# Performance work log

Hardware: AMD Instinct MI355X
Metric: run time of the kernel (lower is better)

## Reference

```python
import jax, jax.numpy as jnp
import numpy as np

N_NODES = 50000
N_EDGES = 600000
BAG = 16
VOCAB = 10000
EMB = 128
HID = 128
N_CLASSES = 10
N_GRAPHS = 512
PAD_IDX = 1


def setup_inputs() -> dict:
    key = jax.random.key(0)
    ks = jax.random.split(key, 12)
    x_tokens = jax.random.randint(ks[0], (N_NODES, BAG), 0, VOCAB)
    src = jax.random.randint(ks[1], (N_EDGES,), 0, N_NODES)
    dst = jax.random.randint(ks[2], (N_EDGES,), 0, N_NODES)
    edge_index = jnp.stack([src, dst])
    batch = jnp.sort(jax.random.randint(ks[3], (N_NODES,), 0, N_GRAPHS))
    # rows 0,1 are zero in the original (weights[2:] filled from pretrained vectors)
    emb_table = (jax.random.normal(ks[4], (VOCAB, EMB)) * 0.02).at[:2].set(0.0)
    s = 1.0 / np.sqrt(EMB)
    w1_l = jax.random.normal(ks[5], (HID, EMB)) * s
    b1 = jnp.zeros((HID,), jnp.float32)
    w1_r = jax.random.normal(ks[6], (HID, EMB)) * s
    w2_l = jax.random.normal(ks[7], (HID, HID)) * s
    b2 = jnp.zeros((HID,), jnp.float32)
    w2_r = jax.random.normal(ks[8], (HID, HID)) * s
    w_out = jax.random.normal(ks[9], (N_CLASSES, HID)) * s
    b_out = jnp.zeros((N_CLASSES,), jnp.float32)
    return {"x_tokens": x_tokens, "edge_index": edge_index, "batch": batch,
            "emb_table": emb_table, "w1_l": w1_l, "b1": b1, "w1_r": w1_r,
            "w2_l": w2_l, "b2": b2, "w2_r": w2_r, "w_out": w_out, "b_out": b_out}


def _embedding_bag_mean(tokens, table):
    # nn.EmbeddingBag mode='mean' with padding_idx: padding tokens excluded from mean
    emb = table[tokens]                                  # [N, BAG, D]
    mask = (tokens != PAD_IDX)[..., None].astype(table.dtype)
    total = jnp.sum(emb * mask, axis=1)                  # [N, D]
    cnt = jnp.clip(jnp.sum(mask, axis=1), 1.0)           # [N, 1]
    return total / cnt


def _sage_conv(x, src, dst, w_l, b_l, w_r):
    # PyG SAGEConv: lin_l(mean_{j in N(i)} x_j) + lin_r(x_i); lin_r has no bias
    n = x.shape[0]
    msg_sum = jax.ops.segment_sum(x[src], dst, num_segments=n)           # [N, D]
    deg = jax.ops.segment_sum(jnp.ones((src.shape[0], 1), x.dtype), dst,
                              num_segments=n)                             # [N, 1]
    aggr = msg_sum / jnp.clip(deg, 1.0)
    return aggr @ w_l.T + b_l + x @ w_r.T


def reference(x_tokens, edge_index, batch, emb_table, w1_l, b1, w1_r,
              w2_l, b2, w2_r, w_out, b_out):
    src, dst = edge_index[0], edge_index[1]
    x = _embedding_bag_mean(x_tokens, emb_table)                 # [N, EMB]
    x = jax.nn.relu(_sage_conv(x, src, dst, w1_l, b1, w1_r))     # [N, HID]
    x = jax.nn.relu(_sage_conv(x, src, dst, w2_l, b2, w2_r))     # [N, HID]
    # global_mean_pool over graph ids
    g_sum = jax.ops.segment_sum(x, batch, num_segments=N_GRAPHS)
    g_cnt = jax.ops.segment_sum(jnp.ones((x.shape[0], 1), x.dtype), batch,
                                num_segments=N_GRAPHS)
    g = g_sum / jnp.clip(g_cnt, 1.0)                             # [G, HID]
    return g @ w_out.T + b_out                                   # [G, C]
```

## Files before the change

### kernel.cpp

```cpp
#include <hip/hip_runtime.h>
#include <hip/hip_bf16.h>

#define NN 50000
#define NE 600000
#define BAG 16
#define EMB 128
#define HID 128
#define NC 10
#define NG 512
#define PAD_IDX 1
#define VOCAB 10000
#define SLOTS 64
#define TPAIRS (VOCAB * EMB / 2)
#define WPAIRS (4 * HID * EMB / 2)
#define CONVB ((TPAIRS + WPAIRS + 255) / 256)
#define NCH1 293
#define RANGES 125
#define RNODES 400
#define CSRB (RANGES * 2)
#define EMVB (NN / 16)
#define NTILES ((NN + 127) / 128)
#define ASTR 40

typedef __attribute__((ext_vector_type(8))) short v8s;
typedef __attribute__((ext_vector_type(4))) float v4f;

__device__ __forceinline__ float bflo(unsigned u) { return __uint_as_float(u << 16); }
__device__ __forceinline__ float bfhi(unsigned u) { return __uint_as_float(u & 0xffff0000u); }
__device__ __forceinline__ unsigned short f2bf(float f) {
    unsigned u = __float_as_uint(f);
    return (unsigned short)((u + 0x7fffu + ((u >> 16) & 1u)) >> 16);
}
__device__ __forceinline__ void acc8(float* a, v8s v) {
    unsigned* u = (unsigned*)&v;
#pragma unroll
    for (int j = 0; j < 4; j++) {
        a[2 * j] += bflo(u[j]);
        a[2 * j + 1] += bfhi(u[j]);
    }
}

__global__ __launch_bounds__(256) void k_conv(const int* __restrict__ src,
                                              const int* __restrict__ dst,
                                              unsigned* __restrict__ queue,
                                              int* __restrict__ qcntG,
                                              const float* __restrict__ t,
                                              unsigned short* __restrict__ tb,
                                              const float* __restrict__ w1l,
                                              const float* __restrict__ w1r,
                                              const float* __restrict__ w2l,
                                              const float* __restrict__ w2r,
                                              unsigned short* __restrict__ wbf,
                                              float* __restrict__ gsum,
                                              float* __restrict__ gcnt,
                                              unsigned short* __restrict__ x0,
                                              unsigned short* __restrict__ x1) {
    __shared__ int qcL[RANGES];
    __shared__ unsigned qbL[RANGES * 64];
    int b = blockIdx.x;
    int tid = threadIdx.x;
    if (b < NCH1) {
        for (int i = tid; i < RANGES; i += 256) qcL[i] = 0;
        __syncthreads();
        int e0 = b * 2048 + tid * 8;
        if (e0 < NE) {
            int4 s0 = *((const int4*)(src + e0));
            int4 s1 = *((const int4*)(src + e0) + 1);
            int4 d0 = *((const int4*)(dst + e0));
            int4 d1 = *((const int4*)(dst + e0) + 1);
            int ss[8] = {s0.x, s0.y, s0.z, s0.w, s1.x, s1.y, s1.z, s1.w};
            int dd[8] = {d0.x, d0.y, d0.z, d0.w, d1.x, d1.y, d1.z, d1.w};
#pragma unroll
            for (int j = 0; j < 8; j++) {
                int q = dd[j] / RNODES;
                unsigned pk = ((unsigned)(dd[j] - q * RNODES) << 16) | (unsigned)ss[j];
                int pos = atomicAdd(&qcL[q], 1);
                if (pos < 64) qbL[q * 64 + pos] = pk;
            }
        }
        __syncthreads();
        if (tid < RANGES) {
            int n = qcL[tid];
            if (n > 64) n = 64;
            qcntG[tid * NCH1 + b] = n;
            unsigned* qp = queue + ((size_t)tid * NCH1 + b) * 64;
            for (int k = 0; k < n; k++) qp[k] = qbL[tid * 64 + k];
        }
        return;
    }
    int i = (b - NCH1) * 256 + tid;
    if (i < NG * HID) gsum[i] = 0.f;
    if (i < NG) gcnt[i] = 0.f;
    if (i < 64) {
        ((unsigned*)(x0 + (size_t)NN * EMB))[i] = 0;
        ((unsigned*)(x1 + (size_t)NN * HID))[i] = 0;
    }
    if (i < TPAIRS) {
        float2 v = *(const float2*)(t + (size_t)i * 2);
        unsigned lo = f2bf(v.x), hi = f2bf(v.y);
        *(unsigned*)(tb + (size_t)i * 2) = lo | (hi << 16);
    } else if (i < TPAIRS + WPAIRS) {
        int j = i - TPAIRS;
        int k = j * 2;
        int arr = k >> 14;
        int o = k & 16383;
        const float* w = (arr == 0) ? w1l : (arr == 1) ? w1r : (arr == 2) ? w2l : w2r;
        float2 v = *(const float2*)(w + o);
        unsigned lo = f2bf(v.x), hi = f2bf(v.y);
        *(unsigned*)(wbf + k) = lo | (hi << 16);
    }
}

__global__ __launch_bounds__(256) void k_scatem(const int* __restrict__ qcntG,
                                                const unsigned* __restrict__ queue,
                                                int* __restrict__ cnt,
                                                unsigned short* __restrict__ slots,
                                                const int* __restrict__ tokens,
                                                const unsigned short* __restrict__ table,
                                                unsigned short* __restrict__ x0) {
    __shared__ int cntL[200];
    __shared__ __align__(16) unsigned short slotsL[200 * SLOTS];
    int b = blockIdx.x;
    int tid = threadIdx.x;
    if (b < CSRB) {
        int r = b >> 1, half = b & 1;
        for (int i = tid; i < 200; i += 256) cntL[i] = 0;
        __syncthreads();
        int dlo = half * 200;
        for (int c = tid; c < NCH1; c += 256) {
            int n = qcntG[r * NCH1 + c];
            const unsigned* qp = queue + ((size_t)r * NCH1 + c) * 64;
            for (int k = 0; k < n; k++) {
                unsigned u = qp[k];
                int d2 = (int)(u >> 16) - dlo;
                if ((unsigned)d2 < 200u) {
                    int p = atomicAdd(&cntL[d2], 1);
                    if (p < SLOTS) slotsL[d2 * SLOTS + p] = (unsigned short)(u & 0xffffu);
                }
            }
        }
        __syncthreads();
        for (int i = tid; i < 200; i += 256) {
            int d = cntL[i];
            if (d > SLOTS) d = SLOTS;
            int d8 = (d + 7) & ~7;
            if (d8 > SLOTS) d8 = SLOTS;
            for (int p = d; p < d8; p++) slotsL[i * SLOTS + p] = (unsigned short)NN;
        }
        __syncthreads();
        int nb = r * RNODES + half * 200;
        uint4* gs = (uint4*)(slots + (size_t)nb * SLOTS);
        const uint4* ls = (const uint4*)slotsL;
        for (int i = tid; i < 200 * SLOTS / 8; i += 256) gs[i] = ls[i];
        for (int i = tid; i < 200; i += 256) cnt[nb + i] = cntL[i];
        return;
    }
    int sl = tid & 15;
    int node = (b - CSRB) * 16 + (tid >> 4);
    const int* tp = tokens + node * BAG;
    int tk[16];
    *(int4*)(tk) = *(const int4*)(tp);
    *(int4*)(tk + 4) = *(const int4*)(tp + 4);
    *(int4*)(tk + 8) = *(const int4*)(tp + 8);
    *(int4*)(tk + 12) = *(const int4*)(tp + 12);
    int c = 0;
#pragma unroll
    for (int t = 0; t < BAG; t++) c += (tk[t] != PAD_IDX);
    float a[8];
#pragma unroll
    for (int j = 0; j < 8; j++) a[j] = 0.f;
    v8s v[16];
#pragma unroll
    for (int t = 0; t < 16; t++)
        v[t] = *(const v8s*)(table + (size_t)tk[t] * EMB + sl * 8);
#pragma unroll
    for (int t = 0; t < 16; t++) acc8(a, v[t]);
    float inv = 1.0f / (float)(c > 0 ? c : 1);
    uint4 o;
    o.x = f2bf(a[0] * inv) | ((unsigned)f2bf(a[1] * inv) << 16);
    o.y = f2bf(a[2] * inv) | ((unsigned)f2bf(a[3] * inv) << 16);
    o.z = f2bf(a[4] * inv) | ((unsigned)f2bf(a[5] * inv) << 16);
    o.w = f2bf(a[6] * inv) | ((unsigned)f2bf(a[7] * inv) << 16);
    *(uint4*)(x0 + (size_t)node * EMB + sl * 8) = o;
}

__global__ __launch_bounds__(256) void k_aggr(const unsigned short* __restrict__ x,
                                              const int* __restrict__ cnt,
                                              const unsigned short* __restrict__ slots,
                                              unsigned short* __restrict__ aggr) {
    int wv = threadIdx.x >> 6;
    int lane = threadIdx.x & 63;
    int n0 = (blockIdx.x * 4 + wv) * 2;
    int n1 = n0 + 1;
    int g = lane >> 4, sl = lane & 15;
    int deg0 = cnt[n0], deg1 = cnt[n1];
    int m0 = deg0 > SLOTS ? SLOTS : deg0;
    int m1 = deg1 > SLOTS ? SLOTS : deg1;
    int m80 = (m0 + 7) & ~7;
    int m81 = (m1 + 7) & ~7;
    int idx0 = slots[(size_t)n0 * SLOTS + lane];
    int idx1 = slots[(size_t)n1 * SLOTS + lane];
    float a0[8], a1[8];
#pragma unroll
    for (int j = 0; j < 8; j++) {
        a0[j] = 0.f;
        a1[j] = 0.f;
    }
    int mm = m80 > m81 ? m80 : m81;
#pragma unroll 2
    for (int i = 0; i < mm; i += 8) {
        bool c0 = (i < m80), c1 = (i < m81);
        v8s w0, w1, w2, w3;
        if (c0) {
            int t00 = __shfl(idx0, i + g, 64);
            int t01 = __shfl(idx0, i + 4 + g, 64);
            w0 = *(const v8s*)(x + (size_t)t00 * HID + sl * 8);
            w1 = *(const v8s*)(x + (size_t)t01 * HID + sl * 8);
        }
        if (c1) {
            int t10 = __shfl(idx1, i + g, 64);
            int t11 = __shfl(idx1, i + 4 + g, 64);
            w2 = *(const v8s*)(x + (size_t)t10 * HID + sl * 8);
            w3 = *(const v8s*)(x + (size_t)t11 * HID + sl * 8);
        }
        if (c0) {
            acc8(a0, w0);
            acc8(a0, w1);
        }
        if (c1) {
            acc8(a1, w2);
            acc8(a1, w3);
        }
    }
#pragma unroll
    for (int j = 0; j < 8; j++) {
        a0[j] += __shfl_xor(a0[j], 16, 64);
        a0[j] += __shfl_xor(a0[j], 32, 64);
        a1[j] += __shfl_xor(a1[j], 16, 64);
        a1[j] += __shfl_xor(a1[j], 32, 64);
    }
    if (g == 0) {
        float inv = 1.0f / (float)(deg0 > 0 ? deg0 : 1);
        uint4 o;
        o.x = f2bf(a0[0] * inv) | ((unsigned)f2bf(a0[1] * inv) << 16);
        o.y = f2bf(a0[2] * inv) | ((unsigned)f2bf(a0[3] * inv) << 16);
        o.z = f2bf(a0[4] * inv) | ((unsigned)f2bf(a0[5] * inv) << 16);
        o.w = f2bf(a0[6] * inv) | ((unsigned)f2bf(a0[7] * inv) << 16);
        *(uint4*)(aggr + (size_t)n0 * HID + sl * 8) = o;
    } else if (g == 1) {
        float inv = 1.0f / (float)(deg1 > 0 ? deg1 : 1);
        uint4 o;
        o.x = f2bf(a1[0] * inv) | ((unsigned)f2bf(a1[1] * inv) << 16);
        o.y = f2bf(a1[2] * inv) | ((unsigned)f2bf(a1[3] * inv) << 16);
        o.z = f2bf(a1[4] * inv) | ((unsigned)f2bf(a1[5] * inv) << 16);
        o.w = f2bf(a1[6] * inv) | ((unsigned)f2bf(a1[7] * inv) << 16);
        *(uint4*)(aggr + (size_t)n1 * HID + sl * 8) = o;
    }
}

__device__ __forceinline__ void sage_kloop(int row0, const unsigned short* __restrict__ xa,
                                           const unsigned short* __restrict__ xr,
                                           const unsigned short* __restrict__ wl,
                                           const unsigned short* __restrict__ wr,
                                           unsigned short* As, unsigned short* Bs,
                                           v4f acc[2][8]) {
    int tid = threadIdx.x;
    int wave = tid >> 6, lane = tid & 63;
    int q = lane >> 4, l16 = lane & 15;
    int r0 = tid >> 2, sg = tid & 3;
    int r1 = (tid + 256) >> 2;
    int gr0 = row0 + r0;
    if (gr0 > NN - 1) gr0 = NN - 1;
    int gr1 = row0 + r1;
    if (gr1 > NN - 1) gr1 = NN - 1;
    v8s ra0 = *(const v8s*)(xa + (size_t)gr0 * HID + sg * 8);
    v8s ra1 = *(const v8s*)(xa + (size_t)gr1 * HID + sg * 8);
    v8s rb0 = *(const v8s*)(wl + (size_t)r0 * HID + sg * 8);
    v8s rb1 = *(const v8s*)(wl + (size_t)r1 * HID + sg * 8);
    for (int kc = 0; kc < 8; kc++) {
        __syncthreads();
        *(v8s*)(As + r0 * ASTR + sg * 8) = ra0;
        *(v8s*)(As + r1 * ASTR + sg * 8) = ra1;
        *(v8s*)(Bs + r0 * ASTR + sg * 8) = rb0;
        *(v8s*)(Bs + r1 * ASTR + sg * 8) = rb1;
        __syncthreads();
        if (kc < 7) {
            int kn = kc + 1;
            const unsigned short* Ag = (kn < 4) ? xa : xr;
            const unsigned short* Bg = (kn < 4) ? wl : wr;
            int koff = (kn & 3) * 32;
            ra0 = *(const v8s*)(Ag + (size_t)gr0 * HID + koff + sg * 8);
            ra1 = *(const v8s*)(Ag + (size_t)gr1 * HID + koff + sg * 8);
            rb0 = *(const v8s*)(Bg + (size_t)r0 * HID + koff + sg * 8);
            rb1 = *(const v8s*)(Bg + (size_t)r1 * HID + koff + sg * 8);
        }
        v8s a0 = *(const v8s*)(As + (wave * 32 + l16) * ASTR + q * 8);
        v8s a1 = *(const v8s*)(As + (wave * 32 + 16 + l16) * ASTR + q * 8);
#pragma unroll
        for (int nt = 0; nt < 8; nt++) {
            v8s b = *(const v8s*)(Bs + (nt * 16 + l16) * ASTR + q * 8);
            acc[0][nt] = __builtin_amdgcn_mfma_f32_16x16x32_bf16(a0, b, acc[0][nt], 0, 0, 0);
            acc[1][nt] = __builtin_amdgcn_mfma_f32_16x16x32_bf16(a1, b, acc[1][nt], 0, 0, 0);
        }
    }
    __syncthreads();
}

__global__ __launch_bounds__(256) void k_sage(const unsigned short* __restrict__ xa,
                                              const unsigned short* __restrict__ xr,
                                              const unsigned short* __restrict__ wl,
                                              const unsigned short* __restrict__ wr,
                                              const float* __restrict__ bias,
                                              unsigned short* __restrict__ out) {
    __shared__ unsigned short As[128 * ASTR];
    __shared__ unsigned short Bs[128 * ASTR];
    int row0 = blockIdx.x * 128;
    v4f acc[2][8];
#pragma unroll
    for (int m = 0; m < 2; m++)
#pragma unroll
        for (int n = 0; n < 8; n++) acc[m][n] = (v4f){0.f, 0.f, 0.f, 0.f};
    sage_kloop(row0, xa, xr, wl, wr, As, Bs, acc);
    int tid = threadIdx.x;
    int wave = tid >> 6, lane = tid & 63;
    int q = lane >> 4, l16 = lane & 15;
#pragma unroll
    for (int nt = 0; nt < 8; nt++) {
        int col = nt * 16 + l16;
        float bv = bias[col];
#pragma unroll
        for (int mt = 0; mt < 2; mt++) {
#pragma unroll
            for (int r = 0; r < 4; r++) {
                int row = row0 + wave * 32 + mt * 16 + q * 4 + r;
                if (row < NN) {
                    float v = acc[mt][nt][r] + bv;
                    v = v > 0.f ? v : 0.f;
                    out[(size_t)row * HID + col] = f2bf(v);
                }
            }
        }
    }
}

__global__ __launch_bounds__(256) void k_sagepool(const unsigned short* __restrict__ xa,
                                                  const unsigned short* __restrict__ xr,
                                                  const unsigned short* __restrict__ wl,
                                                  const unsigned short* __restrict__ wr,
                                                  const float* __restrict__ bias,
                                                  const int* __restrict__ batch,
                                                  float* __restrict__ gsum,
                                                  float* __restrict__ gcnt) {
    __shared__ unsigned short smem[128 * 128];
    unsigned short* As = smem;
    unsigned short* Bs = smem + 128 * ASTR;
    int row0 = blockIdx.x * 128;
    v4f acc[2][8];
#pragma unroll
    for (int m = 0; m < 2; m++)
#pragma unroll
        for (int n = 0; n < 8; n++) acc[m][n] = (v4f){0.f, 0.f, 0.f, 0.f};
    sage_kloop(row0, xa, xr, wl, wr, As, Bs, acc);
    int tid = threadIdx.x;
    int wave = tid >> 6, lane = tid & 63;
    int q = lane >> 4, l16 = lane & 15;
#pragma unroll
    for (int nt = 0; nt < 8; nt++) {
        int col = nt * 16 + l16;
        float bv = bias[col];
#pragma unroll
        for (int mt = 0; mt < 2; mt++) {
#pragma unroll
            for (int r = 0; r < 4; r++) {
                int rl = wave * 32 + mt * 16 + q * 4 + r;
                float v = acc[mt][nt][r] + bv;
                v = v > 0.f ? v : 0.f;
                smem[rl * 128 + col] = f2bf(v);
            }
        }
    }
    __syncthreads();
    if (tid < 128) {
        int col = tid;
        int end = NN - row0;
        if (end > 128) end = 128;
        int cur = batch[row0];
        float acc_p = 0.f;
        int c = 0;
        for (int i = 0; i < end; i++) {
            int b = batch[row0 + i];
            if (b != cur) {
                atomicAdd(&gsum[cur * HID + col], acc_p);
                if (col == 0) atomicAdd(&gcnt[cur], (float)c);
                acc_p = 0.f;
                c = 0;
                cur = b;
            }
            acc_p += __uint_as_float(((unsigned)smem[i * 128 + col]) << 16);
            c++;
        }
        atomicAdd(&gsum[cur * HID + col], acc_p);
        if (col == 0) atomicAdd(&gcnt[cur], (float)c);
    }
}

__global__ __launch_bounds__(128) void k_final(const float* __restrict__ gsum,
                                               const float* __restrict__ gcnt,
                                               const float* __restrict__ w_out,
                                               const float* __restrict__ b_out,
                                               float* __restrict__ out) {
    __shared__ float mean[HID];
    int g = blockIdx.x, tid = threadIdx.x;
    mean[tid] = gsum[g * HID + tid] / fmaxf(gcnt[g], 1.0f);
    __syncthreads();
    if (tid < NC) {
        float s = b_out[tid];
#pragma unroll 16
        for (int d = 0; d < HID; d++) s += mean[d] * w_out[tid * HID + d];
        out[g * NC + tid] = s;
    }
}

extern "C" void kernel_launch(void* const* d_in, const int* in_sizes, int n_in,
                              void* d_out, int out_size, void* d_ws, size_t ws_size,
                              hipStream_t stream) {
    const int* x_tokens = (const int*)d_in[0];
    const int* edge = (const int*)d_in[1];
    const int* batch = (const int*)d_in[2];
    const float* emb_table = (const float*)d_in[3];
    const float* w1l = (const float*)d_in[4];
    const float* b1 = (const float*)d_in[5];
    const float* w1r = (const float*)d_in[6];
    const float* w2l = (const float*)d_in[7];
    const float* b2 = (const float*)d_in[8];
    const float* w2r = (const float*)d_in[9];
    const float* w_out = (const float*)d_in[10];
    const float* b_out = (const float*)d_in[11];
    float* out = (float*)d_out;

    char* ws = (char*)d_ws;
    size_t off = 0;
    auto alloc = [&](size_t bytes) {
        void* p = ws + off;
        off += (bytes + 255) & ~(size_t)255;
        return p;
    };
    int* cnt = (int*)alloc(NN * 4);
    unsigned short* slots = (unsigned short*)alloc((size_t)NN * SLOTS * 2);
    unsigned short* wbf = (unsigned short*)alloc(4 * HID * EMB * 2);
    float* gsum = (float*)alloc(NG * HID * 4);
    float* gcnt = (float*)alloc(NG * 4);
    unsigned short* x0 = (unsigned short*)alloc((size_t)(NN + 1) * EMB * 2);
    unsigned short* x1 = (unsigned short*)alloc((size_t)(NN + 1) * HID * 2);
    unsigned short* aggrb = (unsigned short*)alloc((size_t)NN * HID * 2);
    unsigned* queue = (unsigned*)alloc((size_t)RANGES * NCH1 * 64 * 4);
    int* qcntG = (int*)alloc((size_t)RANGES * NCH1 * 4);
    unsigned short* table_bf = x1;

    const int* srcp = edge;
    const int* dstp = edge + NE;

    k_conv<<<NCH1 + CONVB, 256, 0, stream>>>(srcp, dstp, queue, qcntG, emb_table,
                                             table_bf, w1l, w1r, w2l, w2r, wbf,
                                             gsum, gcnt, x0, x1);
    k_scatem<<<CSRB + EMVB, 256, 0, stream>>>(qcntG, queue, cnt, slots, x_tokens,
                                              table_bf, x0);
    k_aggr<<<NN / 8, 256, 0, stream>>>(x0, cnt, slots, aggrb);
    k_sage<<<NTILES, 256, 0, stream>>>(aggrb, x0, wbf, wbf + 16384, b1, x1);
    k_aggr<<<NN / 8, 256, 0, stream>>>(x1, cnt, slots, aggrb);
    k_sagepool<<<NTILES, 256, 0, stream>>>(aggrb, x1, wbf + 32768, wbf + 49152, b2,
                                           batch, gsum, gcnt);
    k_final<<<NG, 128, 0, stream>>>(gsum, gcnt, w_out, b_out, out);
}
```

Baseline: 195.6 us.

## Fuse all stages into one cooperative persistent kernel with grid syncs

Replaces the seven separate kernel launches with one cooperative persistent kernel. Each stage becomes a device function, blocks loop over its work units in grid-stride order, and the stages are separated by grid-wide syncs. The goal is to remove launch gaps and kernel-boundary drain between the many short stages. The risks are grid-sync overhead, occupancy capped by a fixed 33KB shared allocation and launch bounds of 3, and worse load balance in stages that have few tiles; the multi-kernel path remains as a fallback.

```diff
diff --git a/kernel.cpp b/kernel.cpp
--- a/kernel.cpp
+++ b/kernel.cpp
@@ -1,4 +1,5 @@
 #include <hip/hip_runtime.h>
+#include <hip/hip_cooperative_groups.h>
 #include <hip/hip_bf16.h>
 
 #define NN 50000
@@ -40,124 +41,132 @@
     }
 }
 
-__global__ __launch_bounds__(256) void k_conv(const int* __restrict__ src,
-                                              const int* __restrict__ dst,
-                                              unsigned* __restrict__ queue,
-                                              int* __restrict__ qcntG,
-                                              const float* __restrict__ t,
-                                              unsigned short* __restrict__ tb,
-                                              const float* __restrict__ w1l,
-                                              const float* __restrict__ w1r,
-                                              const float* __restrict__ w2l,
-                                              const float* __restrict__ w2r,
-                                              unsigned short* __restrict__ wbf,
-                                              float* __restrict__ gsum,
-                                              float* __restrict__ gcnt,
-                                              unsigned short* __restrict__ x0,
-                                              unsigned short* __restrict__ x1) {
-    __shared__ int qcL[RANGES];
-    __shared__ unsigned qbL[RANGES * 64];
-    int b = blockIdx.x;
-    int tid = threadIdx.x;
-    if (b < NCH1) {
-        for (int i = tid; i < RANGES; i += 256) qcL[i] = 0;
-        __syncthreads();
-        int e0 = b * 2048 + tid * 8;
-        if (e0 < NE) {
-            int4 s0 = *((const int4*)(src + e0));
-            int4 s1 = *((const int4*)(src + e0) + 1);
-            int4 d0 = *((const int4*)(dst + e0));
-            int4 d1 = *((const int4*)(dst + e0) + 1);
-            int ss[8] = {s0.x, s0.y, s0.z, s0.w, s1.x, s1.y, s1.z, s1.w};
-            int dd[8] = {d0.x, d0.y, d0.z, d0.w, d1.x, d1.y, d1.z, d1.w};
-#pragma unroll
-            for (int j = 0; j < 8; j++) {
-                int q = dd[j] / RNODES;
-                unsigned pk = ((unsigned)(dd[j] - q * RNODES) << 16) | (unsigned)ss[j];
-                int pos = atomicAdd(&qcL[q], 1);
-                if (pos < 64) qbL[q * 64 + pos] = pk;
-            }
-        }
-        __syncthreads();
-        if (tid < RANGES) {
-            int n = qcL[tid];
-            if (n > 64) n = 64;
-            qcntG[tid * NCH1 + b] = n;
-            unsigned* qp = queue + ((size_t)tid * NCH1 + b) * 64;
-            for (int k = 0; k < n; k++) qp[k] = qbL[tid * 64 + k];
-        }
-        return;
-    }
-    int i = (b - NCH1) * 256 + tid;
-    if (i < NG * HID) gsum[i] = 0.f;
-    if (i < NG) gcnt[i] = 0.f;
+struct MegaArgs {
+    const int* src;
+    const int* dst;
+    unsigned* queue;
+    int* qcntG;
+    const float* emb_table;
+    unsigned short* table_bf;
+    const float* w1l;
+    const float* w1r;
+    const float* w2l;
+    const float* w2r;
+    unsigned short* wbf;
+    float* gsum;
+    float* gcnt;
+    unsigned short* x0;
+    unsigned short* x1;
+    unsigned short* aggrb;
+    const int* tokens;
+    int* cnt;
+    unsigned short* slots;
+    const int* batch;
+    const float* b1;
+    const float* b2;
+    const float* w_out;
+    const float* b_out;
+    float* out;
+};
+
+
+__device__ __forceinline__ void bucket_unit(int u, const MegaArgs& A, int* qcL,
+                                            unsigned* qbL) {
+    int tid = threadIdx.x;
+    for (int i = tid; i < RANGES; i += 256) qcL[i] = 0;
+    __syncthreads();
+    int e0 = u * 2048 + tid * 8;
+    if (e0 < NE) {
+        int4 s0 = *((const int4*)(A.src + e0));
+        int4 s1 = *((const int4*)(A.src + e0) + 1);
+        int4 d0 = *((const int4*)(A.dst + e0));
+        int4 d1 = *((const int4*)(A.dst + e0) + 1);
+        int ss[8] = {s0.x, s0.y, s0.z, s0.w, s1.x, s1.y, s1.z, s1.w};
+        int dd[8] = {d0.x, d0.y, d0.z, d0.w, d1.x, d1.y, d1.z, d1.w};
+#pragma unroll
+        for (int j = 0; j < 8; j++) {
+            int q = dd[j] / RNODES;
+            unsigned pk = ((unsigned)(dd[j] - q * RNODES) << 16) | (unsigned)ss[j];
+            int pos = atomicAdd(&qcL[q], 1);
+            if (pos < 64) qbL[q * 64 + pos] = pk;
+        }
+    }
+    __syncthreads();
+    if (tid < RANGES) {
+        int n = qcL[tid];
+        if (n > 64) n = 64;
+        A.qcntG[tid * NCH1 + u] = n;
+        unsigned* qp = A.queue + ((size_t)tid * NCH1 + u) * 64;
+        for (int k = 0; k < n; k++) qp[k] = qbL[tid * 64 + k];
+    }
+    __syncthreads();
+}
+
+__device__ __forceinline__ void conv_unit(int i, const MegaArgs& A) {
+    if (i < NG * HID) A.gsum[i] = 0.f;
+    if (i < NG) A.gcnt[i] = 0.f;
     if (i < 64) {
-        ((unsigned*)(x0 + (size_t)NN * EMB))[i] = 0;
-        ((unsigned*)(x1 + (size_t)NN * HID))[i] = 0;
+        ((unsigned*)(A.x0 + (size_t)NN * EMB))[i] = 0;
+        ((unsigned*)(A.x1 + (size_t)NN * HID))[i] = 0;
     }
     if (i < TPAIRS) {
-        float2 v = *(const float2*)(t + (size_t)i * 2);
+        float2 v = *(const float2*)(A.emb_table + (size_t)i * 2);
         unsigned lo = f2bf(v.x), hi = f2bf(v.y);
-        *(unsigned*)(tb + (size_t)i * 2) = lo | (hi << 16);
+        *(unsigned*)(A.table_bf + (size_t)i * 2) = lo | (hi << 16);
     } else if (i < TPAIRS + WPAIRS) {
         int j = i - TPAIRS;
         int k = j * 2;
         int arr = k >> 14;
         int o = k & 16383;
-        const float* w = (arr == 0) ? w1l : (arr == 1) ? w1r : (arr == 2) ? w2l : w2r;
+        const float* w = (arr == 0) ? A.w1l : (arr == 1) ? A.w1r : (arr == 2) ? A.w2l
+                                                                              : A.w2r;
         float2 v = *(const float2*)(w + o);
         unsigned lo = f2bf(v.x), hi = f2bf(v.y);
-        *(unsigned*)(wbf + k) = lo | (hi << 16);
-    }
-}
-
-__global__ __launch_bounds__(256) void k_scatem(const int* __restrict__ qcntG,
-                                                const unsigned* __restrict__ queue,
-                                                int* __restrict__ cnt,
-                                                unsigned short* __restrict__ slots,
-                                                const int* __restrict__ tokens,
-                                                const unsigned short* __restrict__ table,
-                                                unsigned short* __restrict__ x0) {
-    __shared__ int cntL[200];
-    __shared__ __align__(16) unsigned short slotsL[200 * SLOTS];
-    int b = blockIdx.x;
-    int tid = threadIdx.x;
-    if (b < CSRB) {
-        int r = b >> 1, half = b & 1;
-        for (int i = tid; i < 200; i += 256) cntL[i] = 0;
-        __syncthreads();
-        int dlo = half * 200;
-        for (int c = tid; c < NCH1; c += 256) {
-            int n = qcntG[r * NCH1 + c];
-            const unsigned* qp = queue + ((size_t)r * NCH1 + c) * 64;
-            for (int k = 0; k < n; k++) {
-                unsigned u = qp[k];
-                int d2 = (int)(u >> 16) - dlo;
-                if ((unsigned)d2 < 200u) {
-                    int p = atomicAdd(&cntL[d2], 1);
-                    if (p < SLOTS) slotsL[d2 * SLOTS + p] = (unsigned short)(u & 0xffffu);
-                }
+        *(unsigned*)(A.wbf + k) = lo | (hi << 16);
+    }
+}
+
+__device__ __forceinline__ void csr_unit(int u, const MegaArgs& A, int* cntL,
+                                         unsigned short* slotsL) {
+    int tid = threadIdx.x;
+    int r = u >> 1, half = u & 1;
+    for (int i = tid; i < 200; i += 256) cntL[i] = 0;
+    __syncthreads();
+    int dlo = half * 200;
+    for (int c = tid; c < NCH1; c += 256) {
+        int n = A.qcntG[r * NCH1 + c];
+        const unsigned* qp = A.queue + ((size_t)r * NCH1 + c) * 64;
+        for (int k = 0; k < n; k++) {
+            unsigned v = qp[k];
+            int d2 = (int)(v >> 16) - dlo;
+            if ((unsigned)d2 < 200u) {
+                int p = atomicAdd(&cntL[d2], 1);
+                if (p < SLOTS) slotsL[d2 * SLOTS + p] = (unsigned short)(v & 0xffffu);
             }
         }
-        __syncthreads();
-        for (int i = tid; i < 200; i += 256) {
-            int d = cntL[i];
-            if (d > SLOTS) d = SLOTS;
-            int d8 = (d + 7) & ~7;
-            if (d8 > SLOTS) d8 = SLOTS;
-            for (int p = d; p < d8; p++) slotsL[i * SLOTS + p] = (unsigned short)NN;
-        }
-        __syncthreads();
-        int nb = r * RNODES + half * 200;
-        uint4* gs = (uint4*)(slots + (size_t)nb * SLOTS);
-        const uint4* ls = (const uint4*)slotsL;
-        for (int i = tid; i < 200 * SLOTS / 8; i += 256) gs[i] = ls[i];
-        for (int i = tid; i < 200; i += 256) cnt[nb + i] = cntL[i];
-        return;
-    }
+    }
+    __syncthreads();
+    for (int i = tid; i < 200; i += 256) {
+        int d = cntL[i];
+        if (d > SLOTS) d = SLOTS;
+        int d8 = (d + 7) & ~7;
+        if (d8 > SLOTS) d8 = SLOTS;
+        for (int p = d; p < d8; p++) slotsL[i * SLOTS + p] = (unsigned short)NN;
+    }
+    __syncthreads();
+    int nb = r * RNODES + half * 200;
+    uint4* gs = (uint4*)(A.slots + (size_t)nb * SLOTS);
+    const uint4* ls = (const uint4*)slotsL;
+    for (int i = tid; i < 200 * SLOTS / 8; i += 256) gs[i] = ls[i];
+    for (int i = tid; i < 200; i += 256) A.cnt[nb + i] = cntL[i];
+    __syncthreads();
+}
+
+__device__ __forceinline__ void embed_unit(int u, const MegaArgs& A) {
+    int tid = threadIdx.x;
     int sl = tid & 15;
-    int node = (b - CSRB) * 16 + (tid >> 4);
-    const int* tp = tokens + node * BAG;
+    int node = u * 16 + (tid >> 4);
+    const int* tp = A.tokens + node * BAG;
     int tk[16];
     *(int4*)(tk) = *(const int4*)(tp);
     *(int4*)(tk + 4) = *(const int4*)(tp + 4);
@@ -172,7 +181,7 @@
     v8s v[16];
 #pragma unroll
     for (int t = 0; t < 16; t++)
-        v[t] = *(const v8s*)(table + (size_t)tk[t] * EMB + sl * 8);
+        v[t] = *(const v8s*)(A.table_bf + (size_t)tk[t] * EMB + sl * 8);
 #pragma unroll
     for (int t = 0; t < 16; t++) acc8(a, v[t]);
     float inv = 1.0f / (float)(c > 0 ? c : 1);
@@ -181,18 +190,18 @@
     o.y = f2bf(a[2] * inv) | ((unsigned)f2bf(a[3] * inv) << 16);
     o.z = f2bf(a[4] * inv) | ((unsigned)f2bf(a[5] * inv) << 16);
     o.w = f2bf(a[6] * inv) | ((unsigned)f2bf(a[7] * inv) << 16);
-    *(uint4*)(x0 + (size_t)node * EMB + sl * 8) = o;
-}
-
-__global__ __launch_bounds__(256) void k_aggr(const unsigned short* __restrict__ x,
-                                              const int* __restrict__ cnt,
-                                              const unsigned short* __restrict__ slots,
-                                              unsigned short* __restrict__ aggr) {
+    *(uint4*)(A.x0 + (size_t)node * EMB + sl * 8) = o;
+}
+
+__device__ __forceinline__ void aggr_unit(int u, const unsigned short* __restrict__ x,
+                                          const int* __restrict__ cnt,
+                                          const unsigned short* __restrict__ slots,
+                                          unsigned short* __restrict__ aggr) {
     int wv = threadIdx.x >> 6;
     int lane = threadIdx.x & 63;
-    int n0 = (blockIdx.x * 4 + wv) * 2;
+    int g = lane >> 4, sl = lane & 15;
+    int n0 = (u * 4 + wv) * 2;
     int n1 = n0 + 1;
-    int g = lane >> 4, sl = lane & 15;
     int deg0 = cnt[n0], deg1 = cnt[n1];
     int m0 = deg0 > SLOTS ? SLOTS : deg0;
     int m1 = deg1 > SLOTS ? SLOTS : deg1;
@@ -306,28 +315,22 @@
     __syncthreads();
 }
 
-__global__ __launch_bounds__(256) void k_sage(const unsigned short* __restrict__ xa,
-                                              const unsigned short* __restrict__ xr,
-                                              const unsigned short* __restrict__ wl,
-                                              const unsigned short* __restrict__ wr,
-                                              const float* __restrict__ bias,
-                                              unsigned short* __restrict__ out) {
-    __shared__ unsigned short As[128 * ASTR];
-    __shared__ unsigned short Bs[128 * ASTR];
-    int row0 = blockIdx.x * 128;
+__device__ __forceinline__ void sage1_unit(int u, const MegaArgs& A, unsigned short* As,
+                                           unsigned short* Bs) {
+    int row0 = u * 128;
     v4f acc[2][8];
 #pragma unroll
     for (int m = 0; m < 2; m++)
 #pragma unroll
         for (int n = 0; n < 8; n++) acc[m][n] = (v4f){0.f, 0.f, 0.f, 0.f};
-    sage_kloop(row0, xa, xr, wl, wr, As, Bs, acc);
+    sage_kloop(row0, A.aggrb, A.x0, A.wbf, A.wbf + 16384, As, Bs, acc);
     int tid = threadIdx.x;
     int wave = tid >> 6, lane = tid & 63;
     int q = lane >> 4, l16 = lane & 15;
 #pragma unroll
     for (int nt = 0; nt < 8; nt++) {
         int col = nt * 16 + l16;
-        float bv = bias[col];
+        float bv = A.b1[col];
 #pragma unroll
         for (int mt = 0; mt < 2; mt++) {
 #pragma unroll
@@ -336,38 +339,31 @@
                 if (row < NN) {
                     float v = acc[mt][nt][r] + bv;
                     v = v > 0.f ? v : 0.f;
-                    out[(size_t)row * HID + col] = f2bf(v);
+                    A.x1[(size_t)row * HID + col] = f2bf(v);
                 }
             }
         }
     }
 }
 
-__global__ __launch_bounds__(256) void k_sagepool(const unsigned short* __restrict__ xa,
-                                                  const unsigned short* __restrict__ xr,
-                                                  const unsigned short* __restrict__ wl,
-                                                  const unsigned short* __restrict__ wr,
-                                                  const float* __restrict__ bias,
-                                                  const int* __restrict__ batch,
-                                                  float* __restrict__ gsum,
-                                                  float* __restrict__ gcnt) {
-    __shared__ unsigned short smem[128 * 128];
+__device__ __forceinline__ void sagepool_unit(int u, const MegaArgs& A,
+                                              unsigned short* smem) {
     unsigned short* As = smem;
     unsigned short* Bs = smem + 128 * ASTR;
-    int row0 = blockIdx.x * 128;
+    int row0 = u * 128;
     v4f acc[2][8];
 #pragma unroll
     for (int m = 0; m < 2; m++)
 #pragma unroll
         for (int n = 0; n < 8; n++) acc[m][n] = (v4f){0.f, 0.f, 0.f, 0.f};
-    sage_kloop(row0, xa, xr, wl, wr, As, Bs, acc);
+    sage_kloop(row0, A.aggrb, A.x1, A.wbf + 32768, A.wbf + 49152, As, Bs, acc);
     int tid = threadIdx.x;
     int wave = tid >> 6, lane = tid & 63;
     int q = lane >> 4, l16 = lane & 15;
 #pragma unroll
     for (int nt = 0; nt < 8; nt++) {
         int col = nt * 16 + l16;
-        float bv = bias[col];
+        float bv = A.b2[col];
 #pragma unroll
         for (int mt = 0; mt < 2; mt++) {
 #pragma unroll
@@ -384,14 +380,14 @@
         int col = tid;
         int end = NN - row0;
         if (end > 128) end = 128;
-        int cur = batch[row0];
+        int cur = A.batch[row0];
         float acc_p = 0.f;
         int c = 0;
         for (int i = 0; i < end; i++) {
-            int b = batch[row0 + i];
+            int b = A.batch[row0 + i];
             if (b != cur) {
-                atomicAdd(&gsum[cur * HID + col], acc_p);
-                if (col == 0) atomicAdd(&gcnt[cur], (float)c);
+                atomicAdd(&A.gsum[cur * HID + col], acc_p);
+                if (col == 0) atomicAdd(&A.gcnt[cur], (float)c);
                 acc_p = 0.f;
                 c = 0;
                 cur = b;
@@ -399,45 +395,105 @@
             acc_p += __uint_as_float(((unsigned)smem[i * 128 + col]) << 16);
             c++;
         }
-        atomicAdd(&gsum[cur * HID + col], acc_p);
-        if (col == 0) atomicAdd(&gcnt[cur], (float)c);
-    }
-}
-
-__global__ __launch_bounds__(128) void k_final(const float* __restrict__ gsum,
-                                               const float* __restrict__ gcnt,
-                                               const float* __restrict__ w_out,
-                                               const float* __restrict__ b_out,
-                                               float* __restrict__ out) {
-    __shared__ float mean[HID];
-    int g = blockIdx.x, tid = threadIdx.x;
-    mean[tid] = gsum[g * HID + tid] / fmaxf(gcnt[g], 1.0f);
-    __syncthreads();
-    if (tid < NC) {
-        float s = b_out[tid];
+        atomicAdd(&A.gsum[cur * HID + col], acc_p);
+        if (col == 0) atomicAdd(&A.gcnt[cur], (float)c);
+    }
+    __syncthreads();
+}
+
+__device__ __forceinline__ void final_unit(int u, const MegaArgs& A, float* mean) {
+    int tid = threadIdx.x;
+    __syncthreads();
+    int g = u * 2 + (tid >> 7);
+    int t = tid & 127;
+    mean[tid] = A.gsum[g * HID + t] / fmaxf(A.gcnt[g], 1.0f);
+    __syncthreads();
+    if (t < NC) {
+        float s = A.b_out[t];
+        const float* wo = A.w_out + t * HID;
+        const float* mn = mean + (tid >> 7) * 128;
 #pragma unroll 16
-        for (int d = 0; d < HID; d++) s += mean[d] * w_out[tid * HID + d];
-        out[g * NC + tid] = s;
-    }
+        for (int d = 0; d < HID; d++) s += mn[d] * wo[d];
+        A.out[g * NC + t] = s;
+    }
+}
+
+__global__ __launch_bounds__(256, 3) void k_mega(MegaArgs A) {
+    cooperative_groups::grid_group gg = cooperative_groups::this_grid();
+    __shared__ __align__(16) char SM[33024];
+    int bid = blockIdx.x, gsz = gridDim.x;
+    for (int u = bid; u < NCH1 + CONVB; u += gsz) {
+        if (u < NCH1)
+            bucket_unit(u, A, (int*)SM, (unsigned*)(SM + 512));
+        else
+            conv_unit((u - NCH1) * 256 + threadIdx.x, A);
+    }
+    gg.sync();
+    for (int u = bid; u < CSRB + EMVB; u += gsz) {
+        if (u < CSRB)
+            csr_unit(u, A, (int*)SM, (unsigned short*)(SM + 1024));
+        else
+            embed_unit(u - CSRB, A);
+    }
+    gg.sync();
+    for (int u = bid; u < NN / 8; u += gsz) aggr_unit(u, A.x0, A.cnt, A.slots, A.aggrb);
+    gg.sync();
+    for (int u = bid; u < NTILES; u += gsz)
+        sage1_unit(u, A, (unsigned short*)SM, (unsigned short*)SM + 128 * ASTR);
+    gg.sync();
+    for (int u = bid; u < NN / 8; u += gsz) aggr_unit(u, A.x1, A.cnt, A.slots, A.aggrb);
+    gg.sync();
+    for (int u = bid; u < NTILES; u += gsz) sagepool_unit(u, A, (unsigned short*)SM);
+    gg.sync();
+    for (int u = bid; u < NG / 2; u += gsz) final_unit(u, A, (float*)SM);
+}
+
+__global__ __launch_bounds__(256) void k_conv(MegaArgs A) {
+    __shared__ int qcL[RANGES];
+    __shared__ unsigned qbL[RANGES * 64];
+    int b = blockIdx.x;
+    if (b < NCH1)
+        bucket_unit(b, A, qcL, qbL);
+    else
+        conv_unit((b - NCH1) * 256 + threadIdx.x, A);
+}
+
+__global__ __launch_bounds__(256) void k_scatem(MegaArgs A) {
+    __shared__ int cntL[200];
+    __shared__ __align__(16) unsigned short slotsL[200 * SLOTS];
+    int b = blockIdx.x;
+    if (b < CSRB)
+        csr_unit(b, A, cntL, slotsL);
+    else
+        embed_unit(b - CSRB, A);
+}
+
+__global__ __launch_bounds__(256) void k_aggr(const unsigned short* __restrict__ x,
+                                              const int* __restrict__ cnt,
+                                              const unsigned short* __restrict__ slots,
+                                              unsigned short* __restrict__ aggr) {
+    aggr_unit(blockIdx.x, x, cnt, slots, aggr);
+}
+
+__global__ __launch_bounds__(256) void k_sage(MegaArgs A) {
+    __shared__ unsigned short As[128 * ASTR];
+    __shared__ unsigned short Bs[128 * ASTR];
+    sage1_unit(blockIdx.x, A, As, Bs);
+}
+
+__global__ __launch_bounds__(256) void k_sagepool(MegaArgs A) {
+    __shared__ __align__(16) unsigned short smem[128 * 128];
+    sagepool_unit(blockIdx.x, A, smem);
+}
+
+__global__ __launch_bounds__(256) void k_final(MegaArgs A) {
+    __shared__ float mean[256];
+    final_unit(blockIdx.x, A, mean);
 }
 
 extern "C" void kernel_launch(void* const* d_in, const int* in_sizes, int n_in,
                               void* d_out, int out_size, void* d_ws, size_t ws_size,
                               hipStream_t stream) {
-    const int* x_tokens = (const int*)d_in[0];
-    const int* edge = (const int*)d_in[1];
-    const int* batch = (const int*)d_in[2];
-    const float* emb_table = (const float*)d_in[3];
-    const float* w1l = (const float*)d_in[4];
-    const float* b1 = (const float*)d_in[5];
-    const float* w1r = (const float*)d_in[6];
-    const float* w2l = (const float*)d_in[7];
-    const float* b2 = (const float*)d_in[8];
-    const float* w2r = (const float*)d_in[9];
-    const float* w_out = (const float*)d_in[10];
-    const float* b_out = (const float*)d_in[11];
-    float* out = (float*)d_out;
-
     char* ws = (char*)d_ws;
     size_t off = 0;
     auto alloc = [&](size_t bytes) {
@@ -455,20 +511,53 @@
     unsigned short* aggrb = (unsigned short*)alloc((size_t)NN * HID * 2);
     unsigned* queue = (unsigned*)alloc((size_t)RANGES * NCH1 * 64 * 4);
     int* qcntG = (int*)alloc((size_t)RANGES * NCH1 * 4);
-    unsigned short* table_bf = x1;
-
-    const int* srcp = edge;
-    const int* dstp = edge + NE;
-
-    k_conv<<<NCH1 + CONVB, 256, 0, stream>>>(srcp, dstp, queue, qcntG, emb_table,
-                                             table_bf, w1l, w1r, w2l, w2r, wbf,
-                                             gsum, gcnt, x0, x1);
-    k_scatem<<<CSRB + EMVB, 256, 0, stream>>>(qcntG, queue, cnt, slots, x_tokens,
-                                              table_bf, x0);
-    k_aggr<<<NN / 8, 256, 0, stream>>>(x0, cnt, slots, aggrb);
-    k_sage<<<NTILES, 256, 0, stream>>>(aggrb, x0, wbf, wbf + 16384, b1, x1);
-    k_aggr<<<NN / 8, 256, 0, stream>>>(x1, cnt, slots, aggrb);
-    k_sagepool<<<NTILES, 256, 0, stream>>>(aggrb, x1, wbf + 32768, wbf + 49152, b2,
-                                           batch, gsum, gcnt);
-    k_final<<<NG, 128, 0, stream>>>(gsum, gcnt, w_out, b_out, out);
-}
+
+    MegaArgs h;
+    h.src = (const int*)d_in[1];
+    h.dst = (const int*)d_in[1] + NE;
+    h.queue = queue;
+    h.qcntG = qcntG;
+    h.emb_table = (const float*)d_in[3];
+    h.table_bf = x1;
+    h.w1l = (const float*)d_in[4];
+    h.w1r = (const float*)d_in[6];
+    h.w2l = (const float*)d_in[7];
+    h.w2r = (const float*)d_in[9];
+    h.wbf = wbf;
+    h.gsum = gsum;
+    h.gcnt = gcnt;
+    h.x0 = x0;
+    h.x1 = x1;
+    h.aggrb = aggrb;
+    h.tokens = (const int*)d_in[0];
+    h.cnt = cnt;
+    h.slots = slots;
+    h.batch = (const int*)d_in[2];
+    h.b1 = (const float*)d_in[5];
+    h.b2 = (const float*)d_in[8];
+    h.w_out = (const float*)d_in[10];
+    h.b_out = (const float*)d_in[11];
+    h.out = (float*)d_out;
+
+    bool done = false;
+    int nb = 0;
+    hipError_t qe =
+        hipOccupancyMaxActiveBlocksPerMultiprocessor(&nb, (const void*)k_mega, 256, 0);
+    if (qe == hipSuccess && nb > 0) {
+        int grid = nb * 256;
+        if (grid > 2048) grid = 2048;
+        void* args[] = {&h};
+        if (hipLaunchCooperativeKernel((const void*)k_mega, dim3(grid), dim3(256), args,
+                                       0, stream) == hipSuccess)
+            done = true;
+    }
+    if (!done) {
+        k_conv<<<NCH1 + CONVB, 256, 0, stream>>>(h);
+        k_scatem<<<CSRB + EMVB, 256, 0, stream>>>(h);
+        k_aggr<<<NN / 8, 256, 0, stream>>>(h.x0, h.cnt, h.slots, h.aggrb);
+        k_sage<<<NTILES, 256, 0, stream>>>(h);
+        k_aggr<<<NN / 8, 256, 0, stream>>>(h.x1, h.cnt, h.slots, h.aggrb);
+        k_sagepool<<<NTILES, 256, 0, stream>>>(h);
+        k_final<<<NG / 2, 256, 0, stream>>>(h);
+    }
+}
```

Measured after the change: 510.5 us. 161% more time.
